# Kernel tuning notes

Measured on AMD Instinct MI355X. Metric: run time of the kernel, lower is better.

The kernel has to match this reference:

```python
import jax, jax.numpy as jnp
import numpy as np

B, S, T = 32, 512, 512
SRC_SIZE, TGT_SIZE, OUT_SIZE, NUM_HEAD = 2048, 1024, 1024, 8
HEAD_DIM = OUT_SIZE // NUM_HEAD  # 128


def setup_inputs() -> dict:
    key = jax.random.key(0)
    ks = jax.random.split(key, 12)
    src = jax.random.normal(ks[0], (B, S, SRC_SIZE), dtype=jnp.float32)
    tgt = jax.random.normal(ks[1], (B, T, TGT_SIZE), dtype=jnp.float32)
    # binary float masks (1=valid, 0=pad); guarantee at least one valid src per row
    src_mask = (jax.random.uniform(ks[2], (B, S)) > 0.3).astype(jnp.float32)
    src_mask = src_mask.at[:, 0].set(1.0)
    tgt_mask = (jax.random.uniform(ks[3], (B, T)) > 0.3).astype(jnp.float32)
    tgt_mask = tgt_mask.at[:, 0].set(1.0)
    # FCNet in this repo is weight_norm(Linear) with no activation at drop=0 -> plain Linear
    def lin(k, out_f, in_f):
        return jax.random.normal(k, (out_f, in_f), dtype=jnp.float32) / np.sqrt(in_f)
    W_src = lin(ks[4], 2 * OUT_SIZE, SRC_SIZE)
    b_src = jnp.zeros((2 * OUT_SIZE,), jnp.float32)
    W_tgt = lin(ks[5], OUT_SIZE, TGT_SIZE)
    b_tgt = jnp.zeros((OUT_SIZE,), jnp.float32)
    W_out = lin(ks[6], OUT_SIZE, OUT_SIZE + TGT_SIZE)
    b_out = jnp.zeros((OUT_SIZE,), jnp.float32)
    return {"src": src, "tgt": tgt, "src_mask": src_mask, "tgt_mask": tgt_mask,
            "W_src": W_src, "b_src": b_src, "W_tgt": W_tgt, "b_tgt": b_tgt,
            "W_out": W_out, "b_out": b_out}


def reference(src, tgt, src_mask, tgt_mask, W_src, b_src, W_tgt, b_tgt, W_out, b_out):
    b, s, _ = src.shape
    t = tgt.shape[1]
    # projections (FCNet == Linear here)
    src_trans = jnp.einsum('bsf,of->bso', src, W_src) + b_src        # [B,S,2D]
    tgt_trans = jnp.einsum('btf,of->bto', tgt, W_tgt) + b_tgt        # [B,T,D]
    src_trans = src_trans * src_mask[:, :, None]
    tgt_trans = tgt_trans * tgt_mask[:, :, None]
    src_key, src_val = jnp.split(src_trans, 2, axis=2)               # each [B,S,D]
    # contiguous per-head chunks == reshape
    k = src_key.reshape(b, s, NUM_HEAD, HEAD_DIM)
    v = src_val.reshape(b, s, NUM_HEAD, HEAD_DIM)
    q = tgt_trans.reshape(b, t, NUM_HEAD, HEAD_DIM)
    scores = jnp.einsum('bthd,bshd->bhts', q, k) / np.sqrt(HEAD_DIM)  # [B,H,T,S]
    scores = jnp.where(src_mask[:, None, None, :] == 0, -jnp.inf, scores)
    attn = jax.nn.softmax(scores, axis=-1)
    tgt_update = jnp.einsum('bhts,bshd->bthd', attn, v).reshape(b, t, OUT_SIZE)
    cat_tgt = jnp.concatenate([tgt, tgt_update], axis=2)             # [B,T,TGT+D]
    return jnp.einsum('btf,of->bto', cat_tgt, W_out) + b_out         # [B,T,D]
```

## Files before the change

kernel.cpp:

```cpp
#include <hip/hip_runtime.h>

typedef __attribute__((ext_vector_type(4))) float f32x4;
typedef __attribute__((ext_vector_type(8))) short short8;
typedef unsigned short u16;

__device__ __forceinline__ u16 f2bf(float f) {
  unsigned int u = __float_as_uint(f);
  return (u16)((u + 0x7fffu + ((u >> 16) & 1u)) >> 16);
}

__device__ __forceinline__ void gload16(const void* g, void* l) {
  __builtin_amdgcn_global_load_lds((const __attribute__((address_space(1))) void*)g,
                                   (__attribute__((address_space(3))) void*)l, 16, 0, 0);
}

__global__ void cvt_f32_bf16(const float* __restrict__ in, u16* __restrict__ out, int n4) {
  int i = blockIdx.x * blockDim.x + threadIdx.x;
  int stride = gridDim.x * blockDim.x;
  for (; i < n4; i += stride) {
    float4 v = ((const float4*)in)[i];
    ushort4 o;
    o.x = f2bf(v.x); o.y = f2bf(v.y); o.z = f2bf(v.z); o.w = f2bf(v.w);
    ((ushort4*)out)[i] = o;
  }
}

__global__ void cvt_tgt_strided(const float* __restrict__ in, u16* __restrict__ cat, int n4) {
  int i = blockIdx.x * blockDim.x + threadIdx.x;
  int stride = gridDim.x * blockDim.x;
  for (; i < n4; i += stride) {
    int e = i * 4;
    int row = e >> 10;
    int c = e & 1023;
    float4 v = ((const float4*)in)[i];
    ushort4 o;
    o.x = f2bf(v.x); o.y = f2bf(v.y); o.z = f2bf(v.z); o.w = f2bf(v.w);
    *(ushort4*)(cat + (size_t)row * 2048 + c) = o;
  }
}

template <bool MASK, bool OUTBF, bool VSPLIT>
__global__ __launch_bounds__(512, 2) void gemm256(const u16* __restrict__ A, int lda,
                                                  const u16* __restrict__ W,
                                                  const float* __restrict__ bias,
                                                  const float* __restrict__ rowmask,
                                                  void* __restrict__ Cout, int ldc,
                                                  int nbn, int K,
                                                  u16* __restrict__ vTout) {
  __shared__ __align__(16) u16 lds[3 * 16384];
  const int tid = threadIdx.x;
  const int lane = tid & 63;
  const int wid = tid >> 6;
  const int lr = lane & 15, lh = lane >> 4;
  const int wm = wid >> 2;
  const int wn = wid & 3;

  const int nwg = gridDim.x;
  const int cpx = nwg >> 3;
  const int bid = (blockIdx.x & 7) * cpx + (blockIdx.x >> 3);
  const int bm = bid / nbn;
  const int bn = bid - bm * nbn;

  const u16* Ab = A + (size_t)(bm * 256) * lda;
  const u16* Wb = W + (size_t)(bn * 256) * K;

  const char* gA[2];
  const char* gB[2];
  int ldst[2];
#pragma unroll
  for (int r = 0; r < 2; ++r) {
    int row = r * 128 + (tid >> 2);
    int cb = ((tid & 3) << 4) ^ (((row >> 1) & 3) << 4);
    gA[r] = (const char*)(Ab + (size_t)row * lda) + cb;
    gB[r] = (const char*)(Wb + (size_t)row * K) + cb;
    ldst[r] = r * 8192 + tid * 16;
  }

  auto stageA = [&](int t, int buf) {
    char* d = (char*)lds + buf * 32768;
#pragma unroll
    for (int r = 0; r < 2; ++r) gload16(gA[r] + (size_t)t * 64, d + ldst[r]);
  };
  auto stageB = [&](int t, int buf) {
    char* d = (char*)lds + buf * 32768 + 16384;
#pragma unroll
    for (int r = 0; r < 2; ++r) gload16(gB[r] + (size_t)t * 64, d + ldst[r]);
  };

  const int swz = ((lr >> 1) & 3) << 4;
  const int aoff = (wm * 128 + lr) * 64 + ((lh << 4) ^ swz);
  const int boff = (wn * 64 + lr) * 64 + ((lh << 4) ^ swz);

  f32x4 acc[8][4];
#pragma unroll
  for (int m = 0; m < 8; ++m)
#pragma unroll
    for (int n = 0; n < 4; ++n) acc[m][n] = (f32x4){0.f, 0.f, 0.f, 0.f};

  const int NT = K >> 5;

  stageA(0, 0); stageB(0, 0);
  stageA(1, 1); stageB(1, 1);
  asm volatile("s_waitcnt vmcnt(4)" ::: "memory");
  __builtin_amdgcn_s_barrier();

  int cur = 0;
  for (int t = 0; t < NT; ++t) {
    const char* Al = (const char*)lds + cur * 32768;
    const char* Bl = Al + 16384;
    int nxt = cur + 2; if (nxt >= 3) nxt -= 3;
    const bool pf = (t + 2 < NT);

    short8 bf[4], af[4];
#pragma unroll
    for (int n = 0; n < 4; ++n) bf[n] = *(const short8*)(Bl + boff + n * 1024);
#pragma unroll
    for (int m = 0; m < 4; ++m) af[m] = *(const short8*)(Al + aoff + m * 1024);
    if (pf) stageA(t + 2, nxt);
    __builtin_amdgcn_s_barrier();
    asm volatile("s_waitcnt lgkmcnt(0)" ::: "memory");
    __builtin_amdgcn_sched_barrier(0);
    __builtin_amdgcn_s_setprio(1);
#pragma unroll
    for (int m = 0; m < 4; ++m)
#pragma unroll
      for (int n = 0; n < 4; ++n)
        acc[m][n] = __builtin_amdgcn_mfma_f32_16x16x32_bf16(af[m], bf[n], acc[m][n], 0, 0, 0);
    __builtin_amdgcn_s_setprio(0);
    __builtin_amdgcn_s_barrier();

    short8 af2[4];
#pragma unroll
    for (int m = 0; m < 4; ++m) af2[m] = *(const short8*)(Al + aoff + 4096 + m * 1024);
    if (pf) stageB(t + 2, nxt);
    __builtin_amdgcn_s_barrier();
    asm volatile("s_waitcnt lgkmcnt(0)" ::: "memory");
    __builtin_amdgcn_sched_barrier(0);
    __builtin_amdgcn_s_setprio(1);
#pragma unroll
    for (int m = 0; m < 4; ++m)
#pragma unroll
      for (int n = 0; n < 4; ++n)
        acc[m + 4][n] = __builtin_amdgcn_mfma_f32_16x16x32_bf16(af2[m], bf[n], acc[m + 4][n], 0, 0, 0);
    __builtin_amdgcn_s_setprio(0);
    if (pf) { asm volatile("s_waitcnt vmcnt(4)" ::: "memory"); }
    else    { asm volatile("s_waitcnt vmcnt(0)" ::: "memory"); }
    __builtin_amdgcn_s_barrier();

    cur = cur + 1; if (cur >= 3) cur = 0;
  }

  const int r0 = bm * 256 + wm * 128 + lh * 4;
  const int c0 = bn * 256 + wn * 64 + lr;
  float bv[4];
#pragma unroll
  for (int n = 0; n < 4; ++n) bv[n] = bias[c0 + n * 16];

  if constexpr (VSPLIT) {
    if (c0 >= 1024) {
      const int b = r0 >> 9;
      u16* vrow[4];
#pragma unroll
      for (int n = 0; n < 4; ++n) {
        int vcol = c0 + n * 16 - 1024;
        vrow[n] = vTout + ((size_t)(b * 8 + (vcol >> 7)) * 128 + (vcol & 127)) * 512;
      }
#pragma unroll
      for (int m = 0; m < 8; ++m) {
        float mk[4];
#pragma unroll
        for (int i = 0; i < 4; ++i) mk[i] = rowmask[r0 + m * 16 + i];
        const int s = (r0 + m * 16) & 511;
#pragma unroll
        for (int n = 0; n < 4; ++n) {
          ushort4 o;
          o.x = f2bf((acc[m][n][0] + bv[n]) * mk[0]);
          o.y = f2bf((acc[m][n][1] + bv[n]) * mk[1]);
          o.z = f2bf((acc[m][n][2] + bv[n]) * mk[2]);
          o.w = f2bf((acc[m][n][3] + bv[n]) * mk[3]);
          *(ushort4*)(vrow[n] + s) = o;
        }
      }
      return;
    }
  }

#pragma unroll
  for (int m = 0; m < 8; ++m) {
#pragma unroll
    for (int i = 0; i < 4; ++i) {
      const int row = r0 + m * 16 + i;
      float msk = 1.f;
      if constexpr (MASK) msk = rowmask[row];
#pragma unroll
      for (int n = 0; n < 4; ++n) {
        float v = (acc[m][n][i] + bv[n]) * msk;
        if constexpr (OUTBF)
          ((u16*)Cout)[(size_t)row * ldc + c0 + n * 16] = f2bf(v);
        else
          ((float*)Cout)[(size_t)row * ldc + c0 + n * 16] = v;
      }
    }
  }
}

__global__ __launch_bounds__(256) void attn_fwd(const u16* __restrict__ q,
                                                const u16* __restrict__ kbuf,
                                                const u16* __restrict__ vT,
                                                const float* __restrict__ smask,
                                                u16* __restrict__ cat) {
  __shared__ __align__(16) u16 lds[20480];
  u16* Ks = lds;
  u16* Vt = lds + 8192;
  u16* Ps = lds + 16384;
  const int tid = threadIdx.x;
  const int lane = tid & 63;
  const int w = tid >> 6;
  const int lr = lane & 15, lh = lane >> 4;
  const int bh = blockIdx.x & 255;
  const int qb = blockIdx.x >> 8;
  const int b = bh >> 3;
  const int h = bh & 7;
  const int t0 = qb * 64 + w * 16;
  const float SCALE = 0.08838834764831845f;

  const u16* kbase = kbuf + (size_t)(b * 512) * 1024 + h * 128;
  const u16* vbase = vT + (size_t)bh * 128 * 512;

  short8 qf[4];
  {
    const u16* qp = q + (size_t)(b * 512 + t0 + lr) * 1024 + h * 128 + lh * 8;
#pragma unroll
    for (int kc = 0; kc < 4; ++kc) qf[kc] = *(const short8*)(qp + kc * 32);
  }

  f32x4 o[8];
#pragma unroll
  for (int dt = 0; dt < 8; ++dt) o[dt] = (f32x4){0.f, 0.f, 0.f, 0.f};
  float m_run[4], l_run[4];
#pragma unroll
  for (int i = 0; i < 4; ++i) { m_run[i] = -1e30f; l_run[i] = 0.f; }

  for (int s0 = 0; s0 < 512; s0 += 64) {
    __syncthreads();
#pragma unroll
    for (int it = 0; it < 4; ++it) {
      int idx = it * 256 + tid;
      int kr = idx >> 4, ks = idx & 15;
      gload16(kbase + (size_t)(s0 + kr) * 1024 + ((ks ^ (kr & 7)) * 8), (char*)Ks + idx * 16);
      int vr = idx >> 3, vs = idx & 7;
      gload16(vbase + (size_t)vr * 512 + s0 + ((vs ^ (vr & 7)) * 8), (char*)Vt + idx * 16);
    }
    asm volatile("s_waitcnt vmcnt(0)" ::: "memory");
    __syncthreads();

    f32x4 sc[4];
#pragma unroll
    for (int st = 0; st < 4; ++st) {
      f32x4 c = (f32x4){0.f, 0.f, 0.f, 0.f};
      const int row = st * 16 + lr;
#pragma unroll
      for (int kc = 0; kc < 4; ++kc) {
        short8 kb = *(const short8*)((const char*)Ks + row * 256 +
                                     ((kc * 64 + lh * 16) ^ ((row & 7) << 4)));
        c = __builtin_amdgcn_mfma_f32_16x16x32_bf16(qf[kc], kb, c, 0, 0, 0);
      }
      sc[st] = c;
    }

    float cm[4];
#pragma unroll
    for (int st = 0; st < 4; ++st) cm[st] = smask[b * 512 + s0 + st * 16 + lr];

    float pv[4][4], mx[4];
#pragma unroll
    for (int i = 0; i < 4; ++i) mx[i] = -1e30f;
#pragma unroll
    for (int st = 0; st < 4; ++st)
#pragma unroll
      for (int i = 0; i < 4; ++i) {
        float v = (cm[st] != 0.f) ? sc[st][i] * SCALE : -1e30f;
        pv[st][i] = v;
        mx[i] = fmaxf(mx[i], v);
      }
#pragma unroll
    for (int off = 1; off < 16; off <<= 1)
#pragma unroll
      for (int i = 0; i < 4; ++i) mx[i] = fmaxf(mx[i], __shfl_xor(mx[i], off));

    float m_new[4], scl[4], rs[4];
#pragma unroll
    for (int i = 0; i < 4; ++i) {
      m_new[i] = fmaxf(m_run[i], mx[i]);
      scl[i] = __expf(m_run[i] - m_new[i]);
      rs[i] = 0.f;
    }
#pragma unroll
    for (int st = 0; st < 4; ++st)
#pragma unroll
      for (int i = 0; i < 4; ++i) {
        float p = (cm[st] != 0.f) ? __expf(pv[st][i] - m_new[i]) : 0.f;
        pv[st][i] = p;
        rs[i] += p;
      }
#pragma unroll
    for (int off = 1; off < 16; off <<= 1)
#pragma unroll
      for (int i = 0; i < 4; ++i) rs[i] += __shfl_xor(rs[i], off);
#pragma unroll
    for (int i = 0; i < 4; ++i) {
      l_run[i] = l_run[i] * scl[i] + rs[i];
      m_run[i] = m_new[i];
    }
#pragma unroll
    for (int dt = 0; dt < 8; ++dt)
#pragma unroll
      for (int i = 0; i < 4; ++i) o[dt][i] *= scl[i];

#pragma unroll
    for (int st = 0; st < 4; ++st)
#pragma unroll
      for (int i = 0; i < 4; ++i) {
        const int prow = lh * 4 + i;
        Ps[w * 1024 + prow * 64 + (((st * 2 + (lr >> 3)) ^ (prow & 7)) * 8) + (lr & 7)] =
            f2bf(pv[st][i]);
      }

    short8 pa[2];
#pragma unroll
    for (int s2 = 0; s2 < 2; ++s2)
      pa[s2] = *(const short8*)(Ps + w * 1024 + lr * 64 + (((s2 * 4 + lh) ^ (lr & 7)) * 8));
#pragma unroll
    for (int dt = 0; dt < 8; ++dt) {
#pragma unroll
      for (int s2 = 0; s2 < 2; ++s2) {
        const int row = dt * 16 + lr;
        short8 vb = *(const short8*)((const char*)Vt + row * 128 +
                                     ((s2 * 64 + lh * 16) ^ ((row & 7) << 4)));
        o[dt] = __builtin_amdgcn_mfma_f32_16x16x32_bf16(pa[s2], vb, o[dt], 0, 0, 0);
      }
    }
  }

  float inv[4];
#pragma unroll
  for (int i = 0; i < 4; ++i) inv[i] = 1.f / l_run[i];
  u16* outp = cat + (size_t)(b * 512 + t0 + lh * 4) * 2048 + 1024 + h * 128 + lr;
#pragma unroll
  for (int dt = 0; dt < 8; ++dt)
#pragma unroll
    for (int i = 0; i < 4; ++i)
      outp[(size_t)i * 2048 + dt * 16] = f2bf(o[dt][i] * inv[i]);
}

extern "C" void kernel_launch(void* const* d_in, const int* in_sizes, int n_in,
                              void* d_out, int out_size, void* d_ws, size_t ws_size,
                              hipStream_t stream) {
  (void)in_sizes; (void)n_in; (void)out_size; (void)ws_size;
  const float* src      = (const float*)d_in[0];
  const float* tgt      = (const float*)d_in[1];
  const float* src_mask = (const float*)d_in[2];
  const float* tgt_mask = (const float*)d_in[3];
  const float* W_src    = (const float*)d_in[4];
  const float* b_src    = (const float*)d_in[5];
  const float* W_tgt    = (const float*)d_in[6];
  const float* b_tgt    = (const float*)d_in[7];
  const float* W_out    = (const float*)d_in[8];
  const float* b_out    = (const float*)d_in[9];

  char* ws = (char*)d_ws;
  u16* catb = (u16*)(ws);
  u16* kbuf = (u16*)(ws + 67108864);
  u16* vTb  = (u16*)(ws + 100663296);
  u16* qbuf = (u16*)(ws + 134217728);
  u16* wsrc = (u16*)(ws + 167772160);
  u16* wtgt = (u16*)(ws + 176160768);
  u16* wout = (u16*)(ws + 178257920);

  cvt_f32_bf16<<<2048, 256, 0, stream>>>(src, catb, 16384 * 2048 / 4);
  cvt_f32_bf16<<<1024, 256, 0, stream>>>(W_src, wsrc, 2048 * 2048 / 4);
  cvt_f32_bf16<<<256, 256, 0, stream>>>(W_tgt, wtgt, 1024 * 1024 / 4);
  cvt_f32_bf16<<<512, 256, 0, stream>>>(W_out, wout, 1024 * 2048 / 4);

  gemm256<true, true, true><<<512, 512, 0, stream>>>(catb, 2048, wsrc, b_src, src_mask,
                                                     kbuf, 1024, 8, 2048, vTb);

  cvt_tgt_strided<<<1024, 256, 0, stream>>>(tgt, catb, 16384 * 1024 / 4);

  gemm256<true, true, false><<<256, 512, 0, stream>>>(catb, 2048, wtgt, b_tgt, tgt_mask,
                                                      qbuf, 1024, 4, 1024, nullptr);

  attn_fwd<<<2048, 256, 0, stream>>>(qbuf, kbuf, vTb, src_mask, catb);

  gemm256<false, false, false><<<256, 512, 0, stream>>>(catb, 2048, wout, b_out, nullptr,
                                                        (float*)d_out, 1024, 4, 2048, nullptr);
}
```

Baseline: 411.9 us.

## Restructure GEMM to BK=64 double-buffered quadrant schedule with XOR swizzle

Reworks the 256x256 bf16 GEMM main loop from a triple-buffered BK=32 pipeline into a double-buffered BK=64 pipeline. Each K step is split into four quadrant MFMA phases, with the next tile's A/B halves prefetched between them. Each wave now owns two separated 64x32 sub-blocks instead of one contiguous 128x64 block. The LDS swizzle changes to an 8-way XOR over 128-byte rows, and the launch-bounds occupancy hint of 2 is dropped. The goal is fewer barriers per K unit and better overlap of global loads with MFMA. The cost is 128KB of LDS per block, which likely limits occupancy to one block per CU.

```diff
diff --git a/kernel.cpp b/kernel.cpp
--- a/kernel.cpp
+++ b/kernel.cpp
@@ -40,14 +40,14 @@
 }
 
 template <bool MASK, bool OUTBF, bool VSPLIT>
-__global__ __launch_bounds__(512, 2) void gemm256(const u16* __restrict__ A, int lda,
-                                                  const u16* __restrict__ W,
-                                                  const float* __restrict__ bias,
-                                                  const float* __restrict__ rowmask,
-                                                  void* __restrict__ Cout, int ldc,
-                                                  int nbn, int K,
-                                                  u16* __restrict__ vTout) {
-  __shared__ __align__(16) u16 lds[3 * 16384];
+__global__ __launch_bounds__(512) void gemm256(const u16* __restrict__ A, int lda,
+                                               const u16* __restrict__ W,
+                                               const float* __restrict__ bias,
+                                               const float* __restrict__ rowmask,
+                                               void* __restrict__ Cout, int ldc,
+                                               int nbn, int K,
+                                               u16* __restrict__ vTout) {
+  __shared__ __align__(16) u16 lds[2 * 32768];
   const int tid = threadIdx.x;
   const int lane = tid & 63;
   const int wid = tid >> 6;
@@ -61,35 +61,29 @@
   const int bm = bid / nbn;
   const int bn = bid - bm * nbn;
 
-  const u16* Ab = A + (size_t)(bm * 256) * lda;
-  const u16* Wb = W + (size_t)(bn * 256) * K;
-
-  const char* gA[2];
-  const char* gB[2];
-  int ldst[2];
-#pragma unroll
-  for (int r = 0; r < 2; ++r) {
-    int row = r * 128 + (tid >> 2);
-    int cb = ((tid & 3) << 4) ^ (((row >> 1) & 3) << 4);
-    gA[r] = (const char*)(Ab + (size_t)row * lda) + cb;
-    gB[r] = (const char*)(Wb + (size_t)row * K) + cb;
-    ldst[r] = r * 8192 + tid * 16;
-  }
-
-  auto stageA = [&](int t, int buf) {
-    char* d = (char*)lds + buf * 32768;
-#pragma unroll
-    for (int r = 0; r < 2; ++r) gload16(gA[r] + (size_t)t * 64, d + ldst[r]);
+  const int srow = tid >> 3;
+  const int scol = ((tid & 7) ^ (srow & 7)) << 3;
+  const u16* As0 = A + (size_t)(bm * 256 + srow) * lda + scol;
+  const u16* Ws0 = W + (size_t)(bn * 256 + srow) * K + scol;
+
+  auto stageA = [&](int h, int t, int buf) {
+    char* d = (char*)lds + buf * 65536 + h * 16384 + tid * 16;
+    const u16* s = As0 + (size_t)(h * 128) * lda + t * 64;
+    gload16(s, d);
+    gload16(s + (size_t)64 * lda, d + 8192);
   };
-  auto stageB = [&](int t, int buf) {
-    char* d = (char*)lds + buf * 32768 + 16384;
-#pragma unroll
-    for (int r = 0; r < 2; ++r) gload16(gB[r] + (size_t)t * 64, d + ldst[r]);
+  auto stageB = [&](int h, int t, int buf) {
+    char* d = (char*)lds + buf * 65536 + 32768 + h * 16384 + tid * 16;
+    const u16* s = Ws0 + (size_t)(h * 128) * K + t * 64;
+    gload16(s, d);
+    gload16(s + (size_t)64 * K, d + 8192);
   };
 
-  const int swz = ((lr >> 1) & 3) << 4;
-  const int aoff = (wm * 128 + lr) * 64 + ((lh << 4) ^ swz);
-  const int boff = (wn * 64 + lr) * 64 + ((lh << 4) ^ swz);
+  const int key = (lr & 7) << 4;
+  const int sb0 = ((0 + lh) << 4) ^ key;
+  const int sb1 = ((4 + lh) << 4) ^ key;
+  const int arow = (wm * 64 + lr) * 128;
+  const int brow = 32768 + (wn * 32 + lr) * 128;
 
   f32x4 acc[8][4];
 #pragma unroll
@@ -97,88 +91,130 @@
 #pragma unroll
     for (int n = 0; n < 4; ++n) acc[m][n] = (f32x4){0.f, 0.f, 0.f, 0.f};
 
-  const int NT = K >> 5;
-
-  stageA(0, 0); stageB(0, 0);
-  stageA(1, 1); stageB(1, 1);
+  const int NT = K >> 6;
+
+  stageA(0, 0, 0); stageB(0, 0, 0); stageB(1, 0, 0); stageA(1, 0, 0);
   asm volatile("s_waitcnt vmcnt(4)" ::: "memory");
   __builtin_amdgcn_s_barrier();
-
-  int cur = 0;
+  __builtin_amdgcn_sched_barrier(0);
+
   for (int t = 0; t < NT; ++t) {
-    const char* Al = (const char*)lds + cur * 32768;
-    const char* Bl = Al + 16384;
-    int nxt = cur + 2; if (nxt >= 3) nxt -= 3;
-    const bool pf = (t + 2 < NT);
-
-    short8 bf[4], af[4];
-#pragma unroll
-    for (int n = 0; n < 4; ++n) bf[n] = *(const short8*)(Bl + boff + n * 1024);
-#pragma unroll
-    for (int m = 0; m < 4; ++m) af[m] = *(const short8*)(Al + aoff + m * 1024);
-    if (pf) stageA(t + 2, nxt);
+    const int cur = t & 1, nxt = cur ^ 1;
+    const char* Lb = (const char*)lds + cur * 65536;
+    const bool pf = (t + 1 < NT);
+
+    short8 a[4][2], b0[2][2], b1[2][2];
+
+#pragma unroll
+    for (int m = 0; m < 4; ++m) {
+      a[m][0] = *(const short8*)(Lb + arow + m * 2048 + sb0);
+      a[m][1] = *(const short8*)(Lb + arow + m * 2048 + sb1);
+    }
+#pragma unroll
+    for (int n = 0; n < 2; ++n) {
+      b0[n][0] = *(const short8*)(Lb + brow + n * 2048 + sb0);
+      b0[n][1] = *(const short8*)(Lb + brow + n * 2048 + sb1);
+    }
+    if (pf) stageA(0, t + 1, nxt);
+    asm volatile("s_waitcnt lgkmcnt(0)" ::: "memory");
+    __builtin_amdgcn_sched_barrier(0);
+    __builtin_amdgcn_s_setprio(1);
+#pragma unroll
+    for (int m = 0; m < 4; ++m)
+#pragma unroll
+      for (int n = 0; n < 2; ++n) {
+        acc[m][n] = __builtin_amdgcn_mfma_f32_16x16x32_bf16(a[m][0], b0[n][0], acc[m][n], 0, 0, 0);
+        acc[m][n] = __builtin_amdgcn_mfma_f32_16x16x32_bf16(a[m][1], b0[n][1], acc[m][n], 0, 0, 0);
+      }
+    __builtin_amdgcn_s_setprio(0);
+    if (pf) { asm volatile("s_waitcnt vmcnt(4)" ::: "memory"); }
+    else    { asm volatile("s_waitcnt vmcnt(2)" ::: "memory"); }
     __builtin_amdgcn_s_barrier();
+    __builtin_amdgcn_sched_barrier(0);
+
+#pragma unroll
+    for (int n = 0; n < 2; ++n) {
+      b1[n][0] = *(const short8*)(Lb + brow + 16384 + n * 2048 + sb0);
+      b1[n][1] = *(const short8*)(Lb + brow + 16384 + n * 2048 + sb1);
+    }
+    if (pf) stageB(0, t + 1, nxt);
     asm volatile("s_waitcnt lgkmcnt(0)" ::: "memory");
     __builtin_amdgcn_sched_barrier(0);
     __builtin_amdgcn_s_setprio(1);
 #pragma unroll
     for (int m = 0; m < 4; ++m)
 #pragma unroll
-      for (int n = 0; n < 4; ++n)
-        acc[m][n] = __builtin_amdgcn_mfma_f32_16x16x32_bf16(af[m], bf[n], acc[m][n], 0, 0, 0);
-    __builtin_amdgcn_s_setprio(0);
-    __builtin_amdgcn_s_barrier();
-
-    short8 af2[4];
-#pragma unroll
-    for (int m = 0; m < 4; ++m) af2[m] = *(const short8*)(Al + aoff + 4096 + m * 1024);
-    if (pf) stageB(t + 2, nxt);
-    __builtin_amdgcn_s_barrier();
-    asm volatile("s_waitcnt lgkmcnt(0)" ::: "memory");
-    __builtin_amdgcn_sched_barrier(0);
-    __builtin_amdgcn_s_setprio(1);
-#pragma unroll
-    for (int m = 0; m < 4; ++m)
-#pragma unroll
-      for (int n = 0; n < 4; ++n)
-        acc[m + 4][n] = __builtin_amdgcn_mfma_f32_16x16x32_bf16(af2[m], bf[n], acc[m + 4][n], 0, 0, 0);
+      for (int n = 0; n < 2; ++n) {
+        acc[m][2 + n] = __builtin_amdgcn_mfma_f32_16x16x32_bf16(a[m][0], b1[n][0], acc[m][2 + n], 0, 0, 0);
+        acc[m][2 + n] = __builtin_amdgcn_mfma_f32_16x16x32_bf16(a[m][1], b1[n][1], acc[m][2 + n], 0, 0, 0);
+      }
     __builtin_amdgcn_s_setprio(0);
     if (pf) { asm volatile("s_waitcnt vmcnt(4)" ::: "memory"); }
     else    { asm volatile("s_waitcnt vmcnt(0)" ::: "memory"); }
     __builtin_amdgcn_s_barrier();
-
-    cur = cur + 1; if (cur >= 3) cur = 0;
-  }
-
-  const int r0 = bm * 256 + wm * 128 + lh * 4;
-  const int c0 = bn * 256 + wn * 64 + lr;
-  float bv[4];
-#pragma unroll
-  for (int n = 0; n < 4; ++n) bv[n] = bias[c0 + n * 16];
+    __builtin_amdgcn_sched_barrier(0);
+
+#pragma unroll
+    for (int m = 0; m < 4; ++m) {
+      a[m][0] = *(const short8*)(Lb + 16384 + arow + m * 2048 + sb0);
+      a[m][1] = *(const short8*)(Lb + 16384 + arow + m * 2048 + sb1);
+    }
+    if (pf) stageB(1, t + 1, nxt);
+    asm volatile("s_waitcnt lgkmcnt(0)" ::: "memory");
+    __builtin_amdgcn_sched_barrier(0);
+    __builtin_amdgcn_s_setprio(1);
+#pragma unroll
+    for (int m = 0; m < 4; ++m)
+#pragma unroll
+      for (int n = 0; n < 2; ++n) {
+        acc[4 + m][n] = __builtin_amdgcn_mfma_f32_16x16x32_bf16(a[m][0], b0[n][0], acc[4 + m][n], 0, 0, 0);
+        acc[4 + m][n] = __builtin_amdgcn_mfma_f32_16x16x32_bf16(a[m][1], b0[n][1], acc[4 + m][n], 0, 0, 0);
+      }
+    __builtin_amdgcn_s_setprio(0);
+    if (pf) { asm volatile("s_waitcnt vmcnt(4)" ::: "memory"); }
+    __builtin_amdgcn_s_barrier();
+    __builtin_amdgcn_sched_barrier(0);
+
+    if (pf) stageA(1, t + 1, nxt);
+    __builtin_amdgcn_s_setprio(1);
+#pragma unroll
+    for (int m = 0; m < 4; ++m)
+#pragma unroll
+      for (int n = 0; n < 2; ++n) {
+        acc[4 + m][2 + n] = __builtin_amdgcn_mfma_f32_16x16x32_bf16(a[m][0], b1[n][0], acc[4 + m][2 + n], 0, 0, 0);
+        acc[4 + m][2 + n] = __builtin_amdgcn_mfma_f32_16x16x32_bf16(a[m][1], b1[n][1], acc[4 + m][2 + n], 0, 0, 0);
+      }
+    __builtin_amdgcn_s_setprio(0);
+    if (pf) { asm volatile("s_waitcnt vmcnt(4)" ::: "memory"); }
+    __builtin_amdgcn_s_barrier();
+    __builtin_amdgcn_sched_barrier(0);
+  }
+
+  const int r0 = bm * 256 + wm * 64 + lh * 4;
+  const int c0 = bn * 256 + wn * 32 + lr;
 
   if constexpr (VSPLIT) {
-    if (c0 >= 1024) {
-      const int b = r0 >> 9;
-      u16* vrow[4];
-#pragma unroll
-      for (int n = 0; n < 4; ++n) {
-        int vcol = c0 + n * 16 - 1024;
-        vrow[n] = vTout + ((size_t)(b * 8 + (vcol >> 7)) * 128 + (vcol & 127)) * 512;
-      }
-#pragma unroll
-      for (int m = 0; m < 8; ++m) {
+    if (bn * 256 >= 1024) {
+#pragma unroll
+      for (int mi = 0; mi < 8; ++mi) {
+        const int row_base = r0 + (mi >> 2) * 128 + (mi & 3) * 16;
+        const int b = row_base >> 9;
+        const int s = row_base & 511;
         float mk[4];
 #pragma unroll
-        for (int i = 0; i < 4; ++i) mk[i] = rowmask[r0 + m * 16 + i];
-        const int s = (r0 + m * 16) & 511;
-#pragma unroll
-        for (int n = 0; n < 4; ++n) {
+        for (int i = 0; i < 4; ++i) mk[i] = rowmask[row_base + i];
+#pragma unroll
+        for (int ni = 0; ni < 4; ++ni) {
+          const int col = c0 + (ni >> 1) * 128 + (ni & 1) * 16;
+          const float bv = bias[col];
+          const int vcol = col - 1024;
+          u16* vp = vTout + ((size_t)(b * 8 + (vcol >> 7)) * 128 + (vcol & 127)) * 512 + s;
           ushort4 o;
-          o.x = f2bf((acc[m][n][0] + bv[n]) * mk[0]);
-          o.y = f2bf((acc[m][n][1] + bv[n]) * mk[1]);
-          o.z = f2bf((acc[m][n][2] + bv[n]) * mk[2]);
-          o.w = f2bf((acc[m][n][3] + bv[n]) * mk[3]);
-          *(ushort4*)(vrow[n] + s) = o;
+          o.x = f2bf((acc[mi][ni][0] + bv) * mk[0]);
+          o.y = f2bf((acc[mi][ni][1] + bv) * mk[1]);
+          o.z = f2bf((acc[mi][ni][2] + bv) * mk[2]);
+          o.w = f2bf((acc[mi][ni][3] + bv) * mk[3]);
+          *(ushort4*)vp = o;
         }
       }
       return;
@@ -186,19 +222,21 @@
   }
 
 #pragma unroll
-  for (int m = 0; m < 8; ++m) {
+  for (int mi = 0; mi < 8; ++mi) {
+    const int row_base = r0 + (mi >> 2) * 128 + (mi & 3) * 16;
 #pragma unroll
     for (int i = 0; i < 4; ++i) {
-      const int row = r0 + m * 16 + i;
+      const int row = row_base + i;
       float msk = 1.f;
       if constexpr (MASK) msk = rowmask[row];
 #pragma unroll
-      for (int n = 0; n < 4; ++n) {
-        float v = (acc[m][n][i] + bv[n]) * msk;
+      for (int ni = 0; ni < 4; ++ni) {
+        const int col = c0 + (ni >> 1) * 128 + (ni & 1) * 16;
+        float v = (acc[mi][ni][i] + bias[col]) * msk;
         if constexpr (OUTBF)
-          ((u16*)Cout)[(size_t)row * ldc + c0 + n * 16] = f2bf(v);
+          ((u16*)Cout)[(size_t)row * ldc + col] = f2bf(v);
         else
-          ((float*)Cout)[(size_t)row * ldc + c0 + n * 16] = v;
+          ((float*)Cout)[(size_t)row * ldc + col] = v;
       }
     }
   }
```

Measured after the change: 392.6 us. -4.7%, faster.
